# Performance work log

Hardware: AMD Instinct MI355X
Metric: run time of the kernel (lower is better)

## Reference

```python
import jax, jax.numpy as jnp
import numpy as np

MAX_REL = 16  # block_size//2 = 32//2

def _rel_buckets(T):
    r = jnp.arange(T)
    rel = r[None, :] - r[:, None]              # [T,T] = j - i
    return jnp.clip(rel, -MAX_REL, MAX_REL) + MAX_REL  # [T,T] in [0, 2*MAX_REL]

def setup_inputs() -> dict:
    key = jax.random.key(0)
    ks = jax.random.split(key, 6)
    B, T, C, H = 16, 1024, 64, 64
    x = jax.random.normal(ks[0], (B, T, C), dtype=jnp.float32)
    mask = jnp.tril(jnp.ones((T, T), dtype=jnp.int32))
    Wq = jax.random.normal(ks[1], (C, H), dtype=jnp.float32) * 0.1
    Wk = jax.random.normal(ks[2], (C, H), dtype=jnp.float32) * 0.1
    Wv = jax.random.normal(ks[3], (C, H), dtype=jnp.float32) * 0.1
    rel_key_emb = jax.random.normal(ks[4], (2 * MAX_REL + 1, H), dtype=jnp.float32) * 0.1
    rel_value_emb = jax.random.normal(ks[5], (2 * MAX_REL + 1, H), dtype=jnp.float32) * 0.1
    return {"x": x, "mask": mask, "Wq": Wq, "Wk": Wk, "Wv": Wv,
            "rel_key_emb": rel_key_emb, "rel_value_emb": rel_value_emb}

def reference(x, mask, Wq, Wk, Wv, rel_key_emb, rel_value_emb):
    B, T, C = x.shape
    H = Wq.shape[1]
    scale = H ** -0.5
    q = x @ Wq  # [B,T,H]
    k = x @ Wk
    v = x @ Wv
    buckets = _rel_buckets(T)                 # [T,T] int
    rel_k = rel_key_emb[buckets]              # [T,T,H]
    rel_v = rel_value_emb[buckets]            # [T,T,H]
    content_scores = jnp.einsum('bth,bsh->bts', q, k) * scale     # [B,T,T]
    position_scores = jnp.einsum('bth,tsh->bts', q, rel_k) * scale
    scores = content_scores + position_scores
    scores = jnp.where(mask[None, :, :] == 0, -jnp.inf, scores)
    wei = jax.nn.softmax(scores, axis=-1)     # [B,T,T]  (dropout is identity in eval)
    content_out = jnp.einsum('bts,bsh->bth', wei, v)
    position_out = jnp.einsum('bts,tsh->bth', wei, rel_v)
    return (content_out + position_out, wei)
```

## Files before the change

kernel.cpp:

```cpp
#include <hip/hip_runtime.h>
#include <cstdint>
#include <cstddef>

typedef unsigned short u16;
typedef __attribute__((ext_vector_type(8))) short s16x8;
typedef __attribute__((ext_vector_type(4))) float f32x4;

#define MFMA16(a, b, c) __builtin_amdgcn_mfma_f32_16x16x32_bf16(a, b, c, 0, 0, 0)

#define B_ 16
#define T_ 1024
#define H_ 64
#define SCALE 0.125f

static __device__ __forceinline__ u16 f2bf(float f) {
    unsigned u = __float_as_uint(f);
    u += 0x7FFFu + ((u >> 16) & 1u);
    return (u16)(u >> 16);
}
static __device__ __forceinline__ float bf2f(u16 h) {
    return __uint_as_float((unsigned)h << 16);
}
static __device__ __forceinline__ s16x8 ld8(const u16* p) {
    return *(const s16x8*)p;
}
static __device__ __forceinline__ s16x8 pack8f(const float* p) {
    s16x8 r;
#pragma unroll
    for (int i = 0; i < 8; i++) r[i] = (short)f2bf(p[i]);
    return r;
}

__global__ __launch_bounds__(256) void proj_kernel(
    const float* __restrict__ x, const float* __restrict__ Wq,
    const float* __restrict__ Wk, const float* __restrict__ Wv,
    u16* __restrict__ Qb, u16* __restrict__ Kb, u16* __restrict__ VTb) {
    __shared__ u16 wtb[64][72];
    const int tid = threadIdx.x;
    const int m = blockIdx.y;
    const float* Wm = (m == 0) ? Wq : (m == 1) ? Wk : Wv;
    for (int idx = tid; idx < 1024; idx += 256) {
        const int cin = idx >> 4, c = (idx & 15) << 2;
        const float4 v = *(const float4*)(Wm + cin * 64 + c);
        wtb[c + 0][cin] = f2bf(v.x);
        wtb[c + 1][cin] = f2bf(v.y);
        wtb[c + 2][cin] = f2bf(v.z);
        wtb[c + 3][cin] = f2bf(v.w);
    }
    __syncthreads();
    const int w = tid >> 6, l = tid & 63, lg = l >> 4, lc = l & 15;
    const int base = blockIdx.x * 64 + w * 16;
    const float* xp = x + (size_t)(base + lc) * 64 + lg * 8;
    const s16x8 aX0 = pack8f(xp), aX1 = pack8f(xp + 32);
#pragma unroll
    for (int nt = 0; nt < 4; nt++) {
        const s16x8 b0 = ld8(&wtb[nt * 16 + lc][lg * 8]);
        const s16x8 b1 = ld8(&wtb[nt * 16 + lc][32 + lg * 8]);
        f32x4 acc = {0.f, 0.f, 0.f, 0.f};
        acc = MFMA16(aX0, b0, acc);
        acc = MFMA16(aX1, b1, acc);
        const int col = nt * 16 + lc;
        if (m == 2) {
            const int t0 = base + lg * 4;
            const int bb = t0 >> 10, tl = t0 & 1023;
            ushort4 pk;
            pk.x = f2bf(acc[0]); pk.y = f2bf(acc[1]);
            pk.z = f2bf(acc[2]); pk.w = f2bf(acc[3]);
            *(ushort4*)(VTb + ((size_t)(bb * 64 + col)) * 1024 + tl) = pk;
        } else {
            u16* dst = (m == 0) ? Qb : Kb;
#pragma unroll
            for (int reg = 0; reg < 4; reg++)
                dst[(size_t)(base + lg * 4 + reg) * 64 + col] = f2bf(acc[reg]);
        }
    }
}

__global__ __launch_bounds__(256) void attn_kernel(
    const u16* __restrict__ Qb, const u16* __restrict__ Kb,
    const u16* __restrict__ VTb, const float* __restrict__ rel_key_emb,
    const float* __restrict__ rel_value_emb,
    float* __restrict__ out, float* __restrict__ wei) {
    union EU {
        u16 e[16 * 1024];
        float obuf[4][16][64];
    };
    __shared__ __align__(16) EU sh;
    __shared__ __align__(16) float rv_lds[17][64];
    __shared__ float p_lds[16][33];
    __shared__ float band_lds[16][17];
    __shared__ float sum_lds[4][16];

    const int tid = threadIdx.x, w = tid >> 6, l = tid & 63, lg = l >> 4, lc = l & 15;
    const int bx = blockIdx.x;
    const int s = bx >> 8, i = bx & 255, q = i >> 4;
    const int b = i & 15;
    const int R = (s == 0) ? 63 - q : (s == 1) ? 32 + q : (s == 2) ? 31 - q : q;
    const int wrow = R << 4;
    const int ntiles = R + 1;
    char* eb = (char*)sh.e;

    for (int idx = tid; idx < 17 * 64; idx += 256)
        rv_lds[idx >> 6][idx & 63] = rel_value_emb[idx];
    for (int idx = tid; idx < 16 * 17; idx += 256)
        ((float*)band_lds)[idx] = 0.f;

    const u16* qp = Qb + (size_t)(b * 1024 + wrow + lc) * 64 + lg * 8;
    const s16x8 aQ0 = ld8(qp), aQ1 = ld8(qp + 32);

    if (w == 0) {
#pragma unroll
        for (int nt = 0; nt < 2; nt++) {
            const float* rp = rel_key_emb + (nt * 16 + lc) * 64 + lg * 8;
            const s16x8 b0 = pack8f(rp), b1 = pack8f(rp + 32);
            f32x4 acc = {0.f, 0.f, 0.f, 0.f};
            acc = MFMA16(aQ0, b0, acc);
            acc = MFMA16(aQ1, b1, acc);
#pragma unroll
            for (int reg = 0; reg < 4; reg++)
                p_lds[lg * 4 + reg][nt * 16 + lc] = acc[reg] * SCALE;
        }
    }
    __syncthreads();

    float p0r[4];
#pragma unroll
    for (int reg = 0; reg < 4; reg++) p0r[reg] = p_lds[lg * 4 + reg][0];

    const int P = (ntiles + 1) >> 1;
    const int pq = P >> 2, prem = P & 3;
    const int pstart = w * pq + (w < prem ? w : prem);
    const int pcnt = pq + (w < prem ? 1 : 0);
    const int cbeg = pstart << 1;
    const int cend0 = cbeg + (pcnt << 1);
    const int cend = cend0 < ntiles ? cend0 : ntiles;

    float sum[4] = {0.f, 0.f, 0.f, 0.f};
    f32x4 accO[4];
#pragma unroll
    for (int nt = 0; nt < 4; nt++) accO[nt] = (f32x4){0.f, 0.f, 0.f, 0.f};

    for (int j = 0; j < pcnt; j++) {
        const int sc0 = cbeg + 2 * j;
#pragma unroll
        for (int half = 0; half < 2; half++) {
            const int sc = sc0 + half;
            const int colb = (sc * 16 + lc) * 2;
            if (sc < cend) {
                const u16* kp = Kb + (size_t)(b * 1024 + sc * 16 + lc) * 64 + lg * 8;
                const s16x8 b0 = ld8(kp), b1 = ld8(kp + 32);
                f32x4 acc = {0.f, 0.f, 0.f, 0.f};
                acc = MFMA16(aQ0, b0, acc);
                acc = MFMA16(aQ1, b1, acc);
                const bool bandt = (sc >= ntiles - 2);
#pragma unroll
                for (int reg = 0; reg < 4; reg++) {
                    const int t16 = lg * 4 + reg;
                    const int d = (sc * 16 + lc) - (wrow + t16);
                    float pv = p0r[reg];
                    bool msk = false;
                    if (bandt) {
                        if (d > 0) msk = true;
                        else if (d > -16) pv = p_lds[t16][d + 16];
                    }
                    const float ev = msk ? 0.f : __expf(acc[reg] * SCALE + pv);
                    sum[reg] += ev;
                    *(u16*)(eb + t16 * 2048 + (colb ^ ((t16 & 7) << 4))) = f2bf(ev);
                    if (bandt && d > -16 && d <= 0) band_lds[t16][d + 15] = ev;
                }
            } else {
#pragma unroll
                for (int reg = 0; reg < 4; reg++) {
                    const int t16 = lg * 4 + reg;
                    *(u16*)(eb + t16 * 2048 + (colb ^ ((t16 & 7) << 4))) = 0;
                }
            }
        }
        const int pcolb = sc0 * 32;
        const s16x8 aW =
            *(const s16x8*)(eb + lc * 2048 + ((pcolb + lg * 16) ^ ((lc & 7) << 4)));
#pragma unroll
        for (int nt = 0; nt < 4; nt++) {
            const s16x8 bV =
                ld8(VTb + (size_t)(b * 64 + nt * 16 + lc) * 1024 + sc0 * 16 + lg * 8);
            accO[nt] = MFMA16(aW, bV, accO[nt]);
        }
    }
#pragma unroll
    for (int reg = 0; reg < 4; reg++) {
        sum[reg] += __shfl_xor(sum[reg], 1);
        sum[reg] += __shfl_xor(sum[reg], 2);
        sum[reg] += __shfl_xor(sum[reg], 4);
        sum[reg] += __shfl_xor(sum[reg], 8);
    }
    if (lc == 0) {
#pragma unroll
        for (int reg = 0; reg < 4; reg++) sum_lds[w][lg * 4 + reg] = sum[reg];
    }
    __syncthreads();

    float inv[4];
#pragma unroll
    for (int reg = 0; reg < 4; reg++) {
        const int r = lg * 4 + reg;
        inv[reg] =
            1.0f / (sum_lds[0][r] + sum_lds[1][r] + sum_lds[2][r] + sum_lds[3][r]);
    }
#pragma unroll
    for (int nt = 0; nt < 4; nt++)
#pragma unroll
        for (int reg = 0; reg < 4; reg++) accO[nt][reg] *= inv[reg];

    {
        const int r = tid >> 4;
        const float invr =
            1.0f / (sum_lds[0][r] + sum_lds[1][r] + sum_lds[2][r] + sum_lds[3][r]);
        const int climit = ntiles << 4;
        const int xr = (r & 7) << 4;
        float* wp = wei + ((size_t)b << 20) + (size_t)(wrow + r) * 1024;
        for (int c = (tid & 15) << 2; c < 1024; c += 64) {
            float4 v;
            if (c < climit) {
                const ushort4 ev = *(const ushort4*)(eb + r * 2048 + ((c * 2) ^ xr));
                v.x = bf2f(ev.x) * invr;
                v.y = bf2f(ev.y) * invr;
                v.z = bf2f(ev.z) * invr;
                v.w = bf2f(ev.w) * invr;
            } else {
                v = make_float4(0.f, 0.f, 0.f, 0.f);
            }
            *(float4*)(wp + c) = v;
        }
    }
    __syncthreads();

#pragma unroll
    for (int nt = 0; nt < 4; nt++)
#pragma unroll
        for (int reg = 0; reg < 4; reg++)
            sh.obuf[w][lg * 4 + reg][nt * 16 + lc] = accO[nt][reg];
    __syncthreads();

    {
        const int r = tid >> 4, h = (tid & 15) << 2;
        const float invr =
            1.0f / (sum_lds[0][r] + sum_lds[1][r] + sum_lds[2][r] + sum_lds[3][r]);
        const float4 o0 = *(const float4*)&sh.obuf[0][r][h];
        const float4 o1 = *(const float4*)&sh.obuf[1][r][h];
        const float4 o2 = *(const float4*)&sh.obuf[2][r][h];
        const float4 o3 = *(const float4*)&sh.obuf[3][r][h];
        float a0 = o0.x + o1.x + o2.x + o3.x;
        float a1 = o0.y + o1.y + o2.y + o3.y;
        float a2 = o0.z + o1.z + o2.z + o3.z;
        float a3 = o0.w + o1.w + o2.w + o3.w;
        float bsum = 0.f;
#pragma unroll
        for (int k = 0; k < 16; k++) bsum += band_lds[r][k];
        const float w0 = 1.f - invr * bsum;
        const float4 rv0 = *(const float4*)&rv_lds[0][h];
        a0 += w0 * rv0.x; a1 += w0 * rv0.y; a2 += w0 * rv0.z; a3 += w0 * rv0.w;
#pragma unroll
        for (int k = 0; k < 16; k++) {
            const float bw = band_lds[r][k] * invr;
            const float4 rvk = *(const float4*)&rv_lds[k + 1][h];
            a0 += bw * rvk.x; a1 += bw * rvk.y; a2 += bw * rvk.z; a3 += bw * rvk.w;
        }
        float4 ov; ov.x = a0; ov.y = a1; ov.z = a2; ov.w = a3;
        *(float4*)(out + (size_t)(b * 1024 + wrow + r) * 64 + h) = ov;
    }
}

extern "C" void kernel_launch(void* const* d_in, const int* in_sizes, int n_in,
                              void* d_out, int out_size, void* d_ws, size_t ws_size,
                              hipStream_t stream) {
    const float* x = (const float*)d_in[0];
    const float* Wq = (const float*)d_in[2];
    const float* Wk = (const float*)d_in[3];
    const float* Wv = (const float*)d_in[4];
    const float* rk = (const float*)d_in[5];
    const float* rvv = (const float*)d_in[6];

    float* out = (float*)d_out;
    float* wei = out + (size_t)B_ * T_ * H_;

    u16* Qb = (u16*)d_ws;
    u16* Kb = Qb + (size_t)B_ * T_ * H_;
    u16* VTb = Kb + (size_t)B_ * T_ * H_;

    proj_kernel<<<dim3(256, 3), 256, 0, stream>>>(x, Wq, Wk, Wv, Qb, Kb, VTb);
    attn_kernel<<<dim3(1024), 256, 0, stream>>>(Qb, Kb, VTb, rk, rvv, out, wei);
}
```

Baseline: 39.96 us.

## Prefetch K tiles, early-zero masked wei, LDS atomic PV reduction, nontemporal stores

Several changes at once. The zero upper-triangle region of the weight output is written with nontemporal stores at kernel start, and the next pair of K tiles is register-prefetched while the current pair is scored. The per-wave PV partials are now reduced with LDS atomicAdd into one buffer, which replaces the obuf staging and removes a barrier. rel_value_emb is read from global memory instead of being staged in LDS, and the output and wei stores become nontemporal. This gives more overlap and fewer syncs, at the cost of extra register pressure and LDS atomic contention.

Measured after the change: 53.24 us. 33.2% more time.

```diff
diff --git a/kernel.cpp b/kernel.cpp
--- a/kernel.cpp
+++ b/kernel.cpp
@@ -29,6 +29,11 @@
 #pragma unroll
     for (int i = 0; i < 8; i++) r[i] = (short)f2bf(p[i]);
     return r;
+}
+static __device__ __forceinline__ void slotmap(int bx, int& R, int& b) {
+    const int s = bx >> 8, i = bx & 255, q = i >> 4;
+    b = i & 15;
+    R = (s == 0) ? 63 - q : (s == 1) ? 32 + q : (s == 2) ? 31 - q : q;
 }
 
 __global__ __launch_bounds__(256) void proj_kernel(
@@ -81,51 +86,32 @@
     const u16* __restrict__ VTb, const float* __restrict__ rel_key_emb,
     const float* __restrict__ rel_value_emb,
     float* __restrict__ out, float* __restrict__ wei) {
-    union EU {
-        u16 e[16 * 1024];
-        float obuf[4][16][64];
-    };
-    __shared__ __align__(16) EU sh;
-    __shared__ __align__(16) float rv_lds[17][64];
+    __shared__ __align__(16) char eb[16 * 2048];
+    __shared__ __align__(16) float pvacc[16][64];
     __shared__ float p_lds[16][33];
     __shared__ float band_lds[16][17];
     __shared__ float sum_lds[4][16];
 
     const int tid = threadIdx.x, w = tid >> 6, l = tid & 63, lg = l >> 4, lc = l & 15;
-    const int bx = blockIdx.x;
-    const int s = bx >> 8, i = bx & 255, q = i >> 4;
-    const int b = i & 15;
-    const int R = (s == 0) ? 63 - q : (s == 1) ? 32 + q : (s == 2) ? 31 - q : q;
+    int R, b;
+    slotmap(blockIdx.x, R, b);
     const int wrow = R << 4;
     const int ntiles = R + 1;
-    char* eb = (char*)sh.e;
-
-    for (int idx = tid; idx < 17 * 64; idx += 256)
-        rv_lds[idx >> 6][idx & 63] = rel_value_emb[idx];
-    for (int idx = tid; idx < 16 * 17; idx += 256)
-        ((float*)band_lds)[idx] = 0.f;
+    const int climit = ntiles << 4;
+
+    {
+        const int r = tid >> 4;
+        float* wp = wei + ((size_t)b << 20) + (size_t)(wrow + r) * 1024;
+        const f32x4 zz = {0.f, 0.f, 0.f, 0.f};
+        for (int c = climit + ((tid & 15) << 2); c < 1024; c += 64)
+            __builtin_nontemporal_store(zz, (f32x4*)(wp + c));
+    }
+
+    for (int idx = tid; idx < 16 * 64; idx += 256) ((float*)pvacc)[idx] = 0.f;
+    for (int idx = tid; idx < 16 * 17; idx += 256) ((float*)band_lds)[idx] = 0.f;
 
     const u16* qp = Qb + (size_t)(b * 1024 + wrow + lc) * 64 + lg * 8;
     const s16x8 aQ0 = ld8(qp), aQ1 = ld8(qp + 32);
-
-    if (w == 0) {
-#pragma unroll
-        for (int nt = 0; nt < 2; nt++) {
-            const float* rp = rel_key_emb + (nt * 16 + lc) * 64 + lg * 8;
-            const s16x8 b0 = pack8f(rp), b1 = pack8f(rp + 32);
-            f32x4 acc = {0.f, 0.f, 0.f, 0.f};
-            acc = MFMA16(aQ0, b0, acc);
-            acc = MFMA16(aQ1, b1, acc);
-#pragma unroll
-            for (int reg = 0; reg < 4; reg++)
-                p_lds[lg * 4 + reg][nt * 16 + lc] = acc[reg] * SCALE;
-        }
-    }
-    __syncthreads();
-
-    float p0r[4];
-#pragma unroll
-    for (int reg = 0; reg < 4; reg++) p0r[reg] = p_lds[lg * 4 + reg][0];
 
     const int P = (ntiles + 1) >> 1;
     const int pq = P >> 2, prem = P & 3;
@@ -135,45 +121,84 @@
     const int cend0 = cbeg + (pcnt << 1);
     const int cend = cend0 < ntiles ? cend0 : ntiles;
 
+    s16x8 c00 = {}, c01 = {}, c10 = {}, c11 = {};
+    bool v1 = false;
+    if (pcnt > 0) {
+        const u16* kp0 = Kb + (size_t)(b * 1024 + cbeg * 16 + lc) * 64 + lg * 8;
+        c00 = ld8(kp0);
+        c01 = ld8(kp0 + 32);
+        v1 = (cbeg + 1 < cend);
+        if (v1) { c10 = ld8(kp0 + 1024); c11 = ld8(kp0 + 1024 + 32); }
+    }
+
+    if (w == 0) {
+#pragma unroll
+        for (int nt = 0; nt < 2; nt++) {
+            const float* rp = rel_key_emb + (nt * 16 + lc) * 64 + lg * 8;
+            const s16x8 b0 = pack8f(rp), b1 = pack8f(rp + 32);
+            f32x4 acc = {0.f, 0.f, 0.f, 0.f};
+            acc = MFMA16(aQ0, b0, acc);
+            acc = MFMA16(aQ1, b1, acc);
+#pragma unroll
+            for (int reg = 0; reg < 4; reg++)
+                p_lds[lg * 4 + reg][nt * 16 + lc] = acc[reg] * SCALE;
+        }
+    }
+    __syncthreads();
+
+    float p0r[4];
+#pragma unroll
+    for (int reg = 0; reg < 4; reg++) p0r[reg] = p_lds[lg * 4 + reg][0];
+
     float sum[4] = {0.f, 0.f, 0.f, 0.f};
     f32x4 accO[4];
 #pragma unroll
     for (int nt = 0; nt < 4; nt++) accO[nt] = (f32x4){0.f, 0.f, 0.f, 0.f};
 
+    auto scoreHalf = [&](const s16x8 h0, const s16x8 h1, const int sc) {
+        const int colb = (sc * 16 + lc) * 2;
+        f32x4 acc = {0.f, 0.f, 0.f, 0.f};
+        acc = MFMA16(aQ0, h0, acc);
+        acc = MFMA16(aQ1, h1, acc);
+        const bool bandt = (sc >= ntiles - 2);
+#pragma unroll
+        for (int reg = 0; reg < 4; reg++) {
+            const int t16 = lg * 4 + reg;
+            const int d = (sc * 16 + lc) - (wrow + t16);
+            float pv = p0r[reg];
+            bool msk = false;
+            if (bandt) {
+                if (d > 0) msk = true;
+                else if (d > -16) pv = p_lds[t16][d + 16];
+            }
+            const float ev = msk ? 0.f : __expf(acc[reg] * SCALE + pv);
+            sum[reg] += ev;
+            *(u16*)(eb + t16 * 2048 + (colb ^ ((t16 & 7) << 4))) = f2bf(ev);
+            if (bandt && d > -16 && d <= 0) band_lds[t16][d + 15] = ev;
+        }
+    };
+
     for (int j = 0; j < pcnt; j++) {
         const int sc0 = cbeg + 2 * j;
-#pragma unroll
-        for (int half = 0; half < 2; half++) {
-            const int sc = sc0 + half;
-            const int colb = (sc * 16 + lc) * 2;
-            if (sc < cend) {
-                const u16* kp = Kb + (size_t)(b * 1024 + sc * 16 + lc) * 64 + lg * 8;
-                const s16x8 b0 = ld8(kp), b1 = ld8(kp + 32);
-                f32x4 acc = {0.f, 0.f, 0.f, 0.f};
-                acc = MFMA16(aQ0, b0, acc);
-                acc = MFMA16(aQ1, b1, acc);
-                const bool bandt = (sc >= ntiles - 2);
-#pragma unroll
-                for (int reg = 0; reg < 4; reg++) {
-                    const int t16 = lg * 4 + reg;
-                    const int d = (sc * 16 + lc) - (wrow + t16);
-                    float pv = p0r[reg];
-                    bool msk = false;
-                    if (bandt) {
-                        if (d > 0) msk = true;
-                        else if (d > -16) pv = p_lds[t16][d + 16];
-                    }
-                    const float ev = msk ? 0.f : __expf(acc[reg] * SCALE + pv);
-                    sum[reg] += ev;
-                    *(u16*)(eb + t16 * 2048 + (colb ^ ((t16 & 7) << 4))) = f2bf(ev);
-                    if (bandt && d > -16 && d <= 0) band_lds[t16][d + 15] = ev;
-                }
-            } else {
-#pragma unroll
-                for (int reg = 0; reg < 4; reg++) {
-                    const int t16 = lg * 4 + reg;
-                    *(u16*)(eb + t16 * 2048 + (colb ^ ((t16 & 7) << 4))) = 0;
-                }
+        const s16x8 a00 = c00, a01 = c01, a10 = c10, a11 = c11;
+        const bool va1 = v1;
+        if (j + 1 < pcnt) {
+            const int nsc = sc0 + 2;
+            const u16* kp0 = Kb + (size_t)(b * 1024 + nsc * 16 + lc) * 64 + lg * 8;
+            c00 = ld8(kp0);
+            c01 = ld8(kp0 + 32);
+            v1 = (nsc + 1 < cend);
+            if (v1) { c10 = ld8(kp0 + 1024); c11 = ld8(kp0 + 1024 + 32); }
+        }
+        scoreHalf(a00, a01, sc0);
+        if (va1) {
+            scoreHalf(a10, a11, sc0 + 1);
+        } else {
+            const int colb = ((sc0 + 1) * 16 + lc) * 2;
+#pragma unroll
+            for (int reg = 0; reg < 4; reg++) {
+                const int t16 = lg * 4 + reg;
+                *(u16*)(eb + t16 * 2048 + (colb ^ ((t16 & 7) << 4))) = 0;
             }
         }
         const int pcolb = sc0 * 32;
@@ -197,76 +222,53 @@
 #pragma unroll
         for (int reg = 0; reg < 4; reg++) sum_lds[w][lg * 4 + reg] = sum[reg];
     }
+#pragma unroll
+    for (int nt = 0; nt < 4; nt++)
+#pragma unroll
+        for (int reg = 0; reg < 4; reg++)
+            atomicAdd(&pvacc[lg * 4 + reg][nt * 16 + lc], accO[nt][reg]);
     __syncthreads();
 
-    float inv[4];
-#pragma unroll
-    for (int reg = 0; reg < 4; reg++) {
-        const int r = lg * 4 + reg;
-        inv[reg] =
+    {
+        const int r = tid >> 4, h = (tid & 15) << 2;
+        const float invr =
             1.0f / (sum_lds[0][r] + sum_lds[1][r] + sum_lds[2][r] + sum_lds[3][r]);
-    }
-#pragma unroll
-    for (int nt = 0; nt < 4; nt++)
-#pragma unroll
-        for (int reg = 0; reg < 4; reg++) accO[nt][reg] *= inv[reg];
+        float a0 = pvacc[r][h + 0] * invr;
+        float a1 = pvacc[r][h + 1] * invr;
+        float a2 = pvacc[r][h + 2] * invr;
+        float a3 = pvacc[r][h + 3] * invr;
+        float bsum = 0.f;
+#pragma unroll
+        for (int k = 0; k < 16; k++) bsum += band_lds[r][k];
+        const float w0 = 1.f - invr * bsum;
+        const float4 rv0 = *(const float4*)(rel_value_emb + h);
+        a0 += w0 * rv0.x; a1 += w0 * rv0.y; a2 += w0 * rv0.z; a3 += w0 * rv0.w;
+#pragma unroll
+        for (int k = 0; k < 16; k++) {
+            const float bw = band_lds[r][k] * invr;
+            const float4 rvk = *(const float4*)(rel_value_emb + (k + 1) * 64 + h);
+            a0 += bw * rvk.x; a1 += bw * rvk.y; a2 += bw * rvk.z; a3 += bw * rvk.w;
+        }
+        f32x4 ov; ov[0] = a0; ov[1] = a1; ov[2] = a2; ov[3] = a3;
+        __builtin_nontemporal_store(
+            ov, (f32x4*)(out + (size_t)(b * 1024 + wrow + r) * 64 + h));
+    }
 
     {
         const int r = tid >> 4;
         const float invr =
             1.0f / (sum_lds[0][r] + sum_lds[1][r] + sum_lds[2][r] + sum_lds[3][r]);
-        const int climit = ntiles << 4;
         const int xr = (r & 7) << 4;
         float* wp = wei + ((size_t)b << 20) + (size_t)(wrow + r) * 1024;
-        for (int c = (tid & 15) << 2; c < 1024; c += 64) {
-            float4 v;
-            if (c < climit) {
-                const ushort4 ev = *(const ushort4*)(eb + r * 2048 + ((c * 2) ^ xr));
-                v.x = bf2f(ev.x) * invr;
-                v.y = bf2f(ev.y) * invr;
-                v.z = bf2f(ev.z) * invr;
-                v.w = bf2f(ev.w) * invr;
-            } else {
-                v = make_float4(0.f, 0.f, 0.f, 0.f);
-            }
-            *(float4*)(wp + c) = v;
-        }
-    }
-    __syncthreads();
-
-#pragma unroll
-    for (int nt = 0; nt < 4; nt++)
-#pragma unroll
-        for (int reg = 0; reg < 4; reg++)
-            sh.obuf[w][lg * 4 + reg][nt * 16 + lc] = accO[nt][reg];
-    __syncthreads();
-
-    {
-        const int r = tid >> 4, h = (tid & 15) << 2;
-        const float invr =
-            1.0f / (sum_lds[0][r] + sum_lds[1][r] + sum_lds[2][r] + sum_lds[3][r]);
-        const float4 o0 = *(const float4*)&sh.obuf[0][r][h];
-        const float4 o1 = *(const float4*)&sh.obuf[1][r][h];
-        const float4 o2 = *(const float4*)&sh.obuf[2][r][h];
-        const float4 o3 = *(const float4*)&sh.obuf[3][r][h];
-        float a0 = o0.x + o1.x + o2.x + o3.x;
-        float a1 = o0.y + o1.y + o2.y + o3.y;
-        float a2 = o0.z + o1.z + o2.z + o3.z;
-        float a3 = o0.w + o1.w + o2.w + o3.w;
-        float bsum = 0.f;
-#pragma unroll
-        for (int k = 0; k < 16; k++) bsum += band_lds[r][k];
-        const float w0 = 1.f - invr * bsum;
-        const float4 rv0 = *(const float4*)&rv_lds[0][h];
-        a0 += w0 * rv0.x; a1 += w0 * rv0.y; a2 += w0 * rv0.z; a3 += w0 * rv0.w;
-#pragma unroll
-        for (int k = 0; k < 16; k++) {
-            const float bw = band_lds[r][k] * invr;
-            const float4 rvk = *(const float4*)&rv_lds[k + 1][h];
-            a0 += bw * rvk.x; a1 += bw * rvk.y; a2 += bw * rvk.z; a3 += bw * rvk.w;
-        }
-        float4 ov; ov.x = a0; ov.y = a1; ov.z = a2; ov.w = a3;
-        *(float4*)(out + (size_t)(b * 1024 + wrow + r) * 64 + h) = ov;
+        for (int c = (tid & 15) << 2; c < climit; c += 64) {
+            const ushort4 ev = *(const ushort4*)(eb + r * 2048 + ((c * 2) ^ xr));
+            f32x4 v;
+            v[0] = bf2f(ev.x) * invr;
+            v[1] = bf2f(ev.y) * invr;
+            v[2] = bf2f(ev.z) * invr;
+            v[3] = bf2f(ev.w) * invr;
+            __builtin_nontemporal_store(v, (f32x4*)(wp + c));
+        }
     }
 }
 
```
